# Performance work log

Measured on AMD Instinct MI355X. Metric: run time of the kernel, lower is better.

Reference implementation:

```python
import jax, jax.numpy as jnp
import numpy as np

INPUT_DIM = 1024
K_DIM = 1024
V_DIM = 1024
HEAD = 16
N = 4096


def setup_inputs() -> dict:
    key = jax.random.key(0)
    ks = jax.random.split(key, 6)
    # kaiming_uniform_(a=1): bound = sqrt(6 / ((1+1)*fan_in)) = sqrt(3/fan_in)
    def ku(k, shape):
        fan_in = shape[1]
        b = np.sqrt(3.0 / fan_in)
        return jax.random.uniform(k, shape, jnp.float32, -b, b)
    x = jax.random.normal(ks[0], (1, N, INPUT_DIM), jnp.float32)
    Wq = ku(ks[1], (K_DIM, INPUT_DIM))
    Wk = ku(ks[2], (K_DIM, INPUT_DIM))
    Wv = ku(ks[3], (V_DIM, INPUT_DIM))
    Wo = ku(ks[4], (V_DIM, V_DIM))
    bo = jnp.zeros((V_DIM,), jnp.float32)
    return {"x": x, "Wq": Wq, "Wk": Wk, "Wv": Wv, "Wo": Wo, "bo": bo}


def reference(x, Wq, Wk, Wv, Wo, bo):
    # x: [1, N, C]
    n = x.shape[1]
    hd_k = K_DIM // HEAD
    hd_v = V_DIM // HEAD
    q = jnp.einsum('bnc,kc->bnk', x, Wq).reshape(1, n, HEAD, hd_k).transpose(0, 2, 1, 3)
    k = jnp.einsum('bnc,kc->bnk', x, Wk).reshape(1, n, HEAD, hd_k).transpose(0, 2, 1, 3)
    v = jnp.einsum('bnc,kc->bnk', x, Wv).reshape(1, n, HEAD, hd_v).transpose(0, 2, 1, 3)
    scale = 1.0 / np.sqrt(hd_k).astype(np.float32)
    scores = jnp.einsum('bhqd,bhkd->bhqk', q, k) * scale  # [1,H,N,N]
    attn = jax.nn.softmax(scores, axis=-1)
    ctx = jnp.einsum('bhqk,bhkd->bhqd', attn, v)  # [1,H,N,hd_v]
    ctx = ctx.transpose(0, 2, 1, 3).reshape(1, n, V_DIM)
    out = jnp.einsum('bnv,ov->bno', ctx, Wo) + bo
    return out
```

## Files before the change

### kernel.cpp

```cpp
#include <hip/hip_runtime.h>

typedef short bf16x8 __attribute__((ext_vector_type(8)));
typedef float f32x4 __attribute__((ext_vector_type(4)));
typedef float f32x16 __attribute__((ext_vector_type(16)));
typedef unsigned short u16;
typedef unsigned short u16x8 __attribute__((ext_vector_type(8)));
typedef unsigned int u32;
typedef unsigned int u32x2 __attribute__((ext_vector_type(2)));
typedef unsigned int u32x4 __attribute__((ext_vector_type(4)));

#define MFMA16(a, b, c) __builtin_amdgcn_mfma_f32_16x16x32_bf16((a), (b), (c), 0, 0, 0)
#define MFMA32(a, b, c) __builtin_amdgcn_mfma_f32_32x32x16_bf16((a), (b), (c), 0, 0, 0)

__device__ __forceinline__ u16 f2bf(float f) {
  unsigned u = __builtin_bit_cast(unsigned, f);
  return (u16)((u + 0x7fffu + ((u >> 16) & 1u)) >> 16);
}

__device__ __forceinline__ unsigned cvt_pk_bf16(float lo, float hi) {
  unsigned r;
  asm("v_cvt_pk_bf16_f32 %0, %1, %2" : "=v"(r) : "v"(lo), "v"(hi));
  return r;
}

__device__ __forceinline__ void gload_lds16(const u16* g, u16* lds) {
  __builtin_amdgcn_global_load_lds((__attribute__((address_space(1))) void*)g,
                                   (__attribute__((address_space(3))) void*)lds,
                                   16, 0, 0);
}

__device__ __forceinline__ void publish_barrier() {
  asm volatile("s_waitcnt lgkmcnt(0)" ::: "memory");
  __builtin_amdgcn_sched_barrier(0);
  __builtin_amdgcn_s_barrier();
}

__global__ __launch_bounds__(256) void cvt_all(
    const float* __restrict__ x, const float* __restrict__ w0,
    const float* __restrict__ w1, const float* __restrict__ w2,
    const float* __restrict__ w3, u16* __restrict__ xb, u16* __restrict__ wb) {
  long i = (long)(blockIdx.x * 256 + threadIdx.x) * 8;
  const float* src; u16* dst; long off;
  if (i < 4194304) { src = x; dst = xb; off = i; }
  else {
    long k = i - 4194304; int w = (int)(k >> 20); off = k & 1048575;
    src = (w == 0) ? w0 : (w == 1) ? w1 : (w == 2) ? w2 : w3;
    dst = wb + (long)w * 1048576;
  }
  float4 a = *(const float4*)(src + off);
  float4 b = *(const float4*)(src + off + 4);
  u16x8 o;
  o[0] = f2bf(a.x); o[1] = f2bf(a.y); o[2] = f2bf(a.z); o[3] = f2bf(a.w);
  o[4] = f2bf(b.x); o[5] = f2bf(b.y); o[6] = f2bf(b.z); o[7] = f2bf(b.w);
  *(u16x8*)(dst + off) = o;
}

template <int MODE>
__global__ __launch_bounds__(256) void gemm_bt(
    const u16* __restrict__ A, const u16* __restrict__ Bw,
    u16* __restrict__ Co, float* __restrict__ Cf, const float* __restrict__ bias) {
  constexpr int K = 1024;
  __shared__ u16 As[128 * 32];
  __shared__ u16 Bs[128 * 32];
  const int tid = threadIdx.x, w = tid >> 6, l = tid & 63;
  const int lg = l >> 4, lr = l & 15;
  const int mb = blockIdx.x;
  int mat, nb;
  if (MODE == 0) { mat = blockIdx.y >> 3; nb = blockIdx.y & 7; }
  else           { mat = 0;               nb = blockIdx.y;     }
  const u16* __restrict__ Bp = Bw + (long)mat * 1048576;
  const int wr = w >> 1, wc = w & 1;
  f32x4 acc[4][4] = {};
  const int srow = (l >> 2), scol = (l & 3) * 8;
  for (int kt = 0; kt < K / 32; ++kt) {
    const int kb = kt * 32;
    __syncthreads();
#pragma unroll
    for (int i = 0; i < 2; ++i) {
      int r = w * 32 + i * 16 + srow;
      gload_lds16(A  + (long)(mb * 128 + r) * K + kb + scol, &As[(w * 2 + i) * 512]);
      gload_lds16(Bp + (long)(nb * 128 + r) * K + kb + scol, &Bs[(w * 2 + i) * 512]);
    }
    __syncthreads();
    bf16x8 af[4], bf[4];
#pragma unroll
    for (int m = 0; m < 4; ++m) af[m] = *(const bf16x8*)&As[(wr * 64 + m * 16 + lr) * 32 + lg * 8];
#pragma unroll
    for (int n = 0; n < 4; ++n) bf[n] = *(const bf16x8*)&Bs[(wc * 64 + n * 16 + lr) * 32 + lg * 8];
#pragma unroll
    for (int m = 0; m < 4; ++m)
#pragma unroll
      for (int n = 0; n < 4; ++n)
        acc[m][n] = MFMA16(af[m], bf[n], acc[m][n]);
  }
  const int row0 = mb * 128 + wr * 64, col0 = nb * 128 + wc * 64;
#pragma unroll
  for (int m = 0; m < 4; ++m)
#pragma unroll
    for (int n = 0; n < 4; ++n)
#pragma unroll
      for (int rr = 0; rr < 4; ++rr) {
        int row = row0 + m * 16 + lg * 4 + rr;
        int col = col0 + n * 16 + lr;
        float v = acc[m][n][rr];
        if (MODE == 0) {
          if (mat == 0) v *= 0.18033688011112042f;
          Co[(long)mat * 4194304 + (long)row * 1024 + col] = f2bf(v);
        } else {
          Cf[(long)row * 1024 + col] = v + bias[col];
        }
      }
}

__global__ __launch_bounds__(256) void attn(
    const u16* __restrict__ Qg, const u16* __restrict__ Kg,
    const u16* __restrict__ Vg, u16* __restrict__ Og) {
  __shared__ u16 Ksb[2 * 4096];
  __shared__ u16 Vsb[2 * 64 * 72];
  const int tid = threadIdx.x, w = tid >> 6, l = tid & 63;
  const int l31 = l & 31, hi = l >> 5;

  const int lin = blockIdx.x;
  const int xcd = lin & 7, idx = lin >> 3;
  const int head = xcd * 2 + (idx >> 5), qt = idx & 31;
  const int hb = head * 64;
  const int q0 = qt * 128 + w * 32;

  const u16* __restrict__ Kh = Kg + hb;

  bf16x8 qf[4];
#pragma unroll
  for (int st = 0; st < 4; ++st)
    qf[st] = *(const bf16x8*)&Qg[(long)(q0 + l31) * 1024 + hb + st * 16 + hi * 8];

  f32x16 o0 = {}, o1 = {};
  f32x4 lsv = {};

  const int kr = tid >> 3, c8 = tid & 7;
  const u16* Vgp = Vg + hb + c8 * 8;
  bf16x8 va0, va1;

  const int krow = tid >> 3;
  const int ksrc = (((tid & 7) * 16) ^ ((krow & 7) << 4)) >> 1;
  u16* kdst = Ksb + w * 512;

#define KSTAGE(t_, db_)                                                       \
  {                                                                           \
    gload_lds16(Kh + (long)((t_) * 64 + krow) * 1024 + ksrc,                  \
                kdst + (db_) * 4096);                                         \
    gload_lds16(Kh + (long)((t_) * 64 + 32 + krow) * 1024 + ksrc,             \
                kdst + (db_) * 4096 + 2048);                                  \
  }

#define VLOAD(t_)                                                     \
  {                                                                   \
    long r0_ = (long)(t_) * 64 + kr * 2;                              \
    va0 = *(const bf16x8*)&Vgp[r0_ * 1024];                           \
    va1 = *(const bf16x8*)&Vgp[(r0_ + 1) * 1024];                     \
  }

#define VWRITE(db_)                                                       \
  {                                                                       \
    const int cw = (kr ^ (c8 << 2)) * 2;                                  \
    u16* d_ = Vsb + (db_) * 4608;                                         \
    u32x4 A_ = __builtin_bit_cast(u32x4, va0);                            \
    u32x4 B_ = __builtin_bit_cast(u32x4, va1);                            \
    _Pragma("unroll") for (int dd = 0; dd < 4; ++dd) {                    \
      u32 pe = __builtin_amdgcn_perm(B_[dd], A_[dd], 0x05040100u);        \
      u32 po = __builtin_amdgcn_perm(B_[dd], A_[dd], 0x07060302u);        \
      *(u32*)&d_[(c8 * 8 + 2 * dd) * 72 + cw] = pe;                       \
      *(u32*)&d_[(c8 * 8 + 2 * dd + 1) * 72 + cw] = po;                   \
    }                                                                     \
  }

#define KFRAG(kf_, db_)                                                       \
  {                                                                           \
    _Pragma("unroll") for (int tt = 0; tt < 2; ++tt)                          \
      _Pragma("unroll") for (int st = 0; st < 4; ++st) {                      \
        const int row_ = tt * 32 + l31;                                       \
        const int boff_ = (st * 32 + hi * 16) ^ ((row_ & 7) << 4);            \
        (kf_)[tt][st] =                                                       \
            *(const bf16x8*)&Ksb[(db_) * 4096 + row_ * 64 + (boff_ >> 1)];    \
      }                                                                       \
  }

#define PACKCHUNK(SX, base_, pb_)                                             \
  {                                                                           \
    u32 a0_ = cvt_pk_bf16((SX)[(base_) + 0], (SX)[(base_) + 1]);              \
    u32 b0_ = cvt_pk_bf16((SX)[(base_) + 4], (SX)[(base_) + 5]);              \
    u32 a1_ = cvt_pk_bf16((SX)[(base_) + 2], (SX)[(base_) + 3]);              \
    u32 b1_ = cvt_pk_bf16((SX)[(base_) + 6], (SX)[(base_) + 7]);              \
    u32x2 r0_ = __builtin_amdgcn_permlane32_swap(a0_, b0_, false, false);     \
    u32x2 r1_ = __builtin_amdgcn_permlane32_swap(a1_, b1_, false, false);     \
    u32x4 fv_;                                                                \
    fv_[0] = r0_[0]; fv_[1] = r1_[0]; fv_[2] = r0_[1]; fv_[3] = r1_[1];       \
    (pb_) = __builtin_bit_cast(bf16x8, fv_);                                  \
  }

#define BODY(t_, db_, last_)                                                  \
  {                                                                           \
    if (!(last_)) {                                                           \
      KSTAGE((t_) + 1, (db_) ^ 1);                                            \
      VLOAD((t_) + 1);                                                        \
    }                                                                         \
    bf16x8 kf[2][4];                                                          \
    KFRAG(kf, db_);                                                           \
    f32x16 S0 = {}, S1 = {};                                                  \
    __builtin_amdgcn_s_setprio(1);                                            \
    _Pragma("unroll") for (int st = 0; st < 4; ++st) {                        \
      S0 = MFMA32(kf[0][st], qf[st], S0);                                     \
      S1 = MFMA32(kf[1][st], qf[st], S1);                                     \
    }                                                                         \
    __builtin_amdgcn_s_setprio(0);                                            \
    _Pragma("unroll") for (int r = 0; r < 16; ++r) {                          \
      S0[r] = __builtin_amdgcn_exp2f(S0[r]);                                  \
      S1[r] = __builtin_amdgcn_exp2f(S1[r]);                                  \
    }                                                                         \
    const u16* myV = Vsb + (db_) * 4608;                                      \
    _Pragma("unroll") for (int c = 0; c < 4; ++c) {                           \
      bf16x8 pb;                                                              \
      if (c < 2) { PACKCHUNK(S0, (c & 1) * 8, pb); }                          \
      else       { PACKCHUNK(S1, (c & 1) * 8, pb); }                          \
      const int sw0 = ((8 * c + 4 * hi) ^ (((l31 >> 3) & 7) << 2)) * 2;       \
      const int sw1 = ((8 * c + 4 * hi) ^ ((((l31 + 32) >> 3) & 7) << 2)) * 2;\
      bf16x8 vf0 = *(const bf16x8*)&myV[l31 * 72 + sw0];                      \
      bf16x8 vf1 = *(const bf16x8*)&myV[(32 + l31) * 72 + sw1];               \
      __builtin_amdgcn_s_setprio(1);                                          \
      o0 = MFMA32(vf0, pb, o0);                                               \
      o1 = MFMA32(vf1, pb, o1);                                               \
      __builtin_amdgcn_s_setprio(0);                                          \
    }                                                                         \
    _Pragma("unroll") for (int r2 = 0; r2 < 4; ++r2)                          \
      _Pragma("unroll") for (int j = 0; j < 4; ++j)                           \
        lsv[j] += S0[r2 * 4 + j] + S1[r2 * 4 + j];                            \
    if (!(last_)) VWRITE((db_) ^ 1);                                          \
    publish_barrier();                                                        \
  }

  KSTAGE(0, 0);
  VLOAD(0);
  VWRITE(0);
  asm volatile("s_waitcnt vmcnt(0)" ::: "memory");
  publish_barrier();

  for (int i = 0; i < 32; ++i) {
    BODY(2 * i, 0, false);
    BODY(2 * i + 1, 1, i == 31);
  }

  {
    float sls = (lsv[0] + lsv[1]) + (lsv[2] + lsv[3]);
    float s = sls + __shfl_xor(sls, 32);
    float inv = 1.0f / s;
#pragma unroll
    for (int dt = 0; dt < 2; ++dt) {
#pragma unroll
      for (int r2 = 0; r2 < 4; ++r2) {
        float v0 = dt ? o1[r2 * 4 + 0] : o0[r2 * 4 + 0];
        float v1 = dt ? o1[r2 * 4 + 1] : o0[r2 * 4 + 1];
        float v2 = dt ? o1[r2 * 4 + 2] : o0[r2 * 4 + 2];
        float v3 = dt ? o1[r2 * 4 + 3] : o0[r2 * 4 + 3];
        uint2 pk;
        pk.x = cvt_pk_bf16(v0 * inv, v1 * inv);
        pk.y = cvt_pk_bf16(v2 * inv, v3 * inv);
        const int d0 = dt * 32 + 8 * r2 + 4 * hi;
        *(uint2*)&Og[(long)(q0 + l31) * 1024 + hb + d0] = pk;
      }
    }
  }
#undef KSTAGE
#undef VLOAD
#undef VWRITE
#undef KFRAG
#undef PACKCHUNK
#undef BODY
}

extern "C" void kernel_launch(void* const* d_in, const int* in_sizes, int n_in,
                              void* d_out, int out_size, void* d_ws, size_t ws_size,
                              hipStream_t stream) {
  const float* x  = (const float*)d_in[0];
  const float* Wq = (const float*)d_in[1];
  const float* Wk = (const float*)d_in[2];
  const float* Wv = (const float*)d_in[3];
  const float* Wo = (const float*)d_in[4];
  const float* bo = (const float*)d_in[5];
  float* out = (float*)d_out;

  u16* xb  = (u16*)d_ws;
  u16* wb  = xb + 4194304;
  u16* qkv = wb + 4194304;
  u16* ctx = qkv + 3 * 4194304;

  cvt_all<<<dim3(4096), dim3(256), 0, stream>>>(x, Wq, Wk, Wv, Wo, xb, wb);
  gemm_bt<0><<<dim3(32, 24), dim3(256), 0, stream>>>(xb, wb, qkv, nullptr, nullptr);
  attn<<<dim3(512), dim3(256), 0, stream>>>(qkv, qkv + 4194304, qkv + 8388608, ctx);
  gemm_bt<1><<<dim3(32, 8), dim3(256), 0, stream>>>(ctx, wb + 3 * 1048576, nullptr, out, bo);
}
```

Measured before the change: 167.1 us.

## Software-pipeline attention loop: compute next tile's QK^T before current softmax·V

Restructures the flash-attention inner loop so the QK^T MFMAs for tile t+1 are issued before the exp2, pack and PV MFMAs of tile t. K staging now runs two tiles ahead, with a prologue and an epilogue that peel the first and last tiles. The goal is to overlap the exp/transcendental and pack work with matrix-core work and to hide LDS latency. In exchange it keeps two extra 16-float score accumulators live, which raises VGPR pressure and could lower occupancy or cause spills.

```diff
diff --git a/kernel.cpp b/kernel.cpp
--- a/kernel.cpp
+++ b/kernel.cpp
@@ -184,6 +184,20 @@
       }                                                                       \
   }
 
+#define QKT(S0_, S1_, db_)                                                    \
+  {                                                                           \
+    bf16x8 kf_[2][4];                                                         \
+    KFRAG(kf_, db_);                                                          \
+    S0_ = (f32x16){};                                                         \
+    S1_ = (f32x16){};                                                         \
+    __builtin_amdgcn_s_setprio(1);                                            \
+    _Pragma("unroll") for (int st = 0; st < 4; ++st) {                        \
+      S0_ = MFMA32(kf_[0][st], qf[st], S0_);                                  \
+      S1_ = MFMA32(kf_[1][st], qf[st], S1_);                                  \
+    }                                                                         \
+    __builtin_amdgcn_s_setprio(0);                                            \
+  }
+
 #define PACKCHUNK(SX, base_, pb_)                                             \
   {                                                                           \
     u32 a0_ = cvt_pk_bf16((SX)[(base_) + 0], (SX)[(base_) + 1]);              \
@@ -197,30 +211,17 @@
     (pb_) = __builtin_bit_cast(bf16x8, fv_);                                  \
   }
 
-#define BODY(t_, db_, last_)                                                  \
-  {                                                                           \
-    if (!(last_)) {                                                           \
-      KSTAGE((t_) + 1, (db_) ^ 1);                                            \
-      VLOAD((t_) + 1);                                                        \
-    }                                                                         \
-    bf16x8 kf[2][4];                                                          \
-    KFRAG(kf, db_);                                                           \
-    f32x16 S0 = {}, S1 = {};                                                  \
-    __builtin_amdgcn_s_setprio(1);                                            \
-    _Pragma("unroll") for (int st = 0; st < 4; ++st) {                        \
-      S0 = MFMA32(kf[0][st], qf[st], S0);                                     \
-      S1 = MFMA32(kf[1][st], qf[st], S1);                                     \
-    }                                                                         \
-    __builtin_amdgcn_s_setprio(0);                                            \
+#define FINISH(SC0, SC1, db_)                                                 \
+  {                                                                           \
     _Pragma("unroll") for (int r = 0; r < 16; ++r) {                          \
-      S0[r] = __builtin_amdgcn_exp2f(S0[r]);                                  \
-      S1[r] = __builtin_amdgcn_exp2f(S1[r]);                                  \
+      SC0[r] = __builtin_amdgcn_exp2f(SC0[r]);                                \
+      SC1[r] = __builtin_amdgcn_exp2f(SC1[r]);                                \
     }                                                                         \
     const u16* myV = Vsb + (db_) * 4608;                                      \
     _Pragma("unroll") for (int c = 0; c < 4; ++c) {                           \
       bf16x8 pb;                                                              \
-      if (c < 2) { PACKCHUNK(S0, (c & 1) * 8, pb); }                          \
-      else       { PACKCHUNK(S1, (c & 1) * 8, pb); }                          \
+      if (c < 2) { PACKCHUNK(SC0, (c & 1) * 8, pb); }                         \
+      else       { PACKCHUNK(SC1, (c & 1) * 8, pb); }                         \
       const int sw0 = ((8 * c + 4 * hi) ^ (((l31 >> 3) & 7) << 2)) * 2;       \
       const int sw1 = ((8 * c + 4 * hi) ^ ((((l31 + 32) >> 3) & 7) << 2)) * 2;\
       bf16x8 vf0 = *(const bf16x8*)&myV[l31 * 72 + sw0];                      \
@@ -232,21 +233,43 @@
     }                                                                         \
     _Pragma("unroll") for (int r2 = 0; r2 < 4; ++r2)                          \
       _Pragma("unroll") for (int j = 0; j < 4; ++j)                           \
-        lsv[j] += S0[r2 * 4 + j] + S1[r2 * 4 + j];                            \
-    if (!(last_)) VWRITE((db_) ^ 1);                                          \
-    publish_barrier();                                                        \
-  }
+        lsv[j] += SC0[r2 * 4 + j] + SC1[r2 * 4 + j];                          \
+  }
+
+  f32x16 Sa0, Sa1, Sb0, Sb1;
 
   KSTAGE(0, 0);
   VLOAD(0);
+  asm volatile("s_waitcnt vmcnt(0)" ::: "memory");
+  publish_barrier();
+  QKT(Sa0, Sa1, 0);
+  KSTAGE(1, 1);
   VWRITE(0);
   asm volatile("s_waitcnt vmcnt(0)" ::: "memory");
   publish_barrier();
 
-  for (int i = 0; i < 32; ++i) {
-    BODY(2 * i, 0, false);
-    BODY(2 * i + 1, 1, i == 31);
-  }
+#define BODY(t_, db_, SC0, SC1, SN0, SN1)                                     \
+  {                                                                           \
+    KSTAGE((t_) + 2, db_);                                                    \
+    VLOAD((t_) + 1);                                                          \
+    QKT(SN0, SN1, (db_) ^ 1);                                                 \
+    FINISH(SC0, SC1, db_);                                                    \
+    VWRITE((db_) ^ 1);                                                        \
+    publish_barrier();                                                        \
+  }
+
+  for (int i = 0; i < 31; ++i) {
+    BODY(2 * i, 0, Sa0, Sa1, Sb0, Sb1);
+    BODY(2 * i + 1, 1, Sb0, Sb1, Sa0, Sa1);
+  }
+  {
+    VLOAD(63);
+    QKT(Sb0, Sb1, 1);
+    FINISH(Sa0, Sa1, 0);
+    VWRITE(1);
+    publish_barrier();
+  }
+  FINISH(Sb0, Sb1, 1);
 
   {
     float sls = (lsv[0] + lsv[1]) + (lsv[2] + lsv[3]);
@@ -272,7 +295,9 @@
 #undef VLOAD
 #undef VWRITE
 #undef KFRAG
+#undef QKT
 #undef PACKCHUNK
+#undef FINISH
 #undef BODY
 }
 
```

New measurement: 161.1 us. 1.04x faster.
